# Kernel optimization log

Hardware: AMD Instinct MI355X
Metric: run time of the kernel (lower is better)

## Reference

```python
import jax, jax.numpy as jnp
import numpy as np


def _conv(x, w):
    # SpykeTorch snn.Convolution: plain conv2d, no bias, no padding (VALID)
    return jax.lax.conv_general_dilated(
        x, w, window_strides=(1, 1), padding='VALID',
        dimension_numbers=('NCHW', 'OIHW', 'NCHW'))


def _pad2(x, p=2):
    # sf.pad(input, pad=(2,2,2,2), value=0): zero-pad last two (spatial) dims
    return jnp.pad(x, ((0, 0), (0, 0), (p, p), (p, p)))


def _fire(pot, thr):
    # sf.fire: thresholded[pot <= thr] = 0 ; spk = thresholded.sign()
    thresholded = jnp.where(pot > thr, pot, jnp.zeros((), pot.dtype))
    spk = (pot > thr).astype(pot.dtype)
    return spk, thresholded


def _pool(x, k, s):
    # sf.pooling: max_pool2d, floor mode (== VALID reduce_window)
    return jax.lax.reduce_window(
        x, -jnp.inf, jax.lax.max,
        window_dimensions=(1, 1, k, k),
        window_strides=(1, 1, s, s),
        padding='VALID')


def setup_inputs() -> dict:
    key = jax.random.key(0)
    kx, k1, k2, k3 = jax.random.split(key, 4)
    # (T, C, H, W): T timesteps act as batch in SpykeTorch
    x = jax.random.uniform(kx, (20, 6, 160, 160), dtype=jnp.float32)

    def xavier_normal(k, shape):
        fan_in = shape[1] * shape[2] * shape[3]
        fan_out = shape[0] * shape[2] * shape[3]
        std = float(np.sqrt(2.0 / (fan_in + fan_out)))
        return jax.random.normal(k, shape, dtype=jnp.float32) * std

    w1 = xavier_normal(k1, (30, 6, 4, 4))
    w2 = xavier_normal(k2, (250, 30, 3, 3))
    w3 = xavier_normal(k3, (200, 250, 3, 3))
    return {'x': x, 'w1': w1, 'w2': w2, 'w3': w3, 'layer_idx': 3}


def reference(x, w1, w2, w3, layer_idx):
    # Eval-mode forward path of deepSNN up to `layer_idx` (tensor-returning branches)
    CONV1_T, CONV2_T, CONV3_T = 1.0, 1.0, 25.0
    inp = _pad2(x.astype(jnp.float32))          # (T,6,164,164)
    pot = _conv(inp, w1)                        # (T,30,161,161)
    spk, pot = _fire(pot, CONV1_T)
    if layer_idx == 1:
        return spk, pot
    pot = _conv(_pad2(_pool(spk, 2, 2)), w2)    # (T,250,82,82)
    spk, pot = _fire(pot, CONV2_T)
    if layer_idx == 2:
        return spk, pot
    pot = _conv(_pad2(_pool(spk, 3, 3)), w3)    # (T,200,29,29)
    spk, pot = _fire(pot, CONV3_T)
    return spk, pot
```

## Files before the change

kernel.cpp:

```cpp
#include <hip/hip_runtime.h>
#include <hip/hip_bf16.h>


#define OUT_HALF 3364000
#define MASK_PLANE 128000
#define T_FLOATS 168200

typedef float f32x16 __attribute__((ext_vector_type(16)));
typedef short bf8s __attribute__((ext_vector_type(8)));
typedef float f32x4 __attribute__((ext_vector_type(4)));
typedef f32x4 f32x4u __attribute__((aligned(4)));

static __device__ __forceinline__ unsigned int pkbf(float a, float b) {
    union { __hip_bfloat162 h; unsigned int u; } cv;
    cv.h = __float22bfloat162_rn(make_float2(a, b));
    return cv.u;
}
static __device__ __forceinline__ unsigned short bfbits(float a) {
    union { __hip_bfloat16 h; unsigned short u; } cv;
    cv.h = __float2bfloat16(a);
    return cv.u;
}

__global__ __launch_bounds__(256) void k_prep(const float* __restrict__ x,
                                              const float* __restrict__ w2,
                                              float* __restrict__ xpad,
                                              float* __restrict__ w2t,
                                              unsigned int* __restrict__ flags2) {
    int bidx = blockIdx.x;
    int tid = threadIdx.x;
    if (bidx >= 1576) {
        int tb = bidx - 1576;
        if (tb == 0)
            for (int i = tid; i < 540; i += 256) flags2[i] = 0u;
        int idx = tb * 256 + tid;
        if (idx < 67500) {
            int oc = idx / 270, ck = idx % 270;
            w2t[ck * 250 + oc] = w2[idx];
        }
        return;
    }
    for (int e = bidx * 256 + tid; e < 3227520; e += 403456) {
        int tc = e / 26896;
        int rem = e - tc * 26896;
        int r = rem / 164, col = rem - r * 164;
        int sr = r - 2, sc = col - 2;
        float v = 0.f;
        if ((unsigned)sr < 160u && (unsigned)sc < 160u)
            v = x[(tc * 160 + sr) * 160 + sc];
        xpad[e] = v;
    }
}

__global__ __launch_bounds__(256) void k_conv1m(const float* __restrict__ xpad,
                                                const float* __restrict__ w1,
                                                unsigned int* __restrict__ mask1) {
    __shared__ unsigned short B_lds[6 * 64 * 8];

    int tid = threadIdx.x;
#pragma unroll
    for (int n = 0; n < 12; ++n) {
        int q = n * 256 + tid;
        int i = q & 7, ll = (q >> 3) & 63, ks = q >> 9;
        int oc = ll & 31;
        int kg = ks * 16 + ((ll >> 5) << 3) + i;
        float w = (oc < 30) ? w1[oc * 96 + kg] : 0.f;
        B_lds[q] = bfbits(w);
    }
    __syncthreads();

    int l = tid & 63, wv = tid >> 6;
    int b = blockIdx.x;
    int t = b / 100;
    int u = (b % 100) * 4 + wv;
    int pr = u / 5, jblk = u % 5;
    int m = l & 31, hi = l >> 5;
    int j = jblk * 32 + m;

    bf8s bq[6];
#pragma unroll
    for (int ks = 0; ks < 6; ++ks)
        bq[ks] = *(const bf8s*)&B_lds[(ks * 64 + l) * 8];

    f32x16 acc0 = (f32x16)(0.0f);
    f32x16 acc1 = (f32x16)(0.0f);
    int r0 = 2 * pr + 2 * hi;

#pragma unroll
    for (int ks = 0; ks < 6; ++ks) {
        const float* base = xpad + ((t * 6 + ks) * 164 + r0) * 164 + j;
        f32x4 v0 = *(const f32x4u*)(base);
        f32x4 v1 = *(const f32x4u*)(base + 164);
        f32x4 v2 = *(const f32x4u*)(base + 328);
        union { bf8s s; unsigned int u4[4]; } a0, a1;
        a0.u4[0] = pkbf(v0.x, v0.y);
        a0.u4[1] = pkbf(v0.z, v0.w);
        a0.u4[2] = pkbf(v1.x, v1.y);
        a0.u4[3] = pkbf(v1.z, v1.w);
        a1.u4[0] = a0.u4[2];
        a1.u4[1] = a0.u4[3];
        a1.u4[2] = pkbf(v2.x, v2.y);
        a1.u4[3] = pkbf(v2.z, v2.w);
        acc0 = __builtin_amdgcn_mfma_f32_32x32x16_bf16(a0.s, bq[ks], acc0, 0, 0, 0);
        acc1 = __builtin_amdgcn_mfma_f32_32x32x16_bf16(a1.s, bq[ks], acc1, 0, 0, 0);
    }

    unsigned int mbase = (unsigned int)((t * 80 + pr) * 80 + jblk * 16);
#pragma unroll
    for (int a = 0; a < 8; ++a) {
        bool s = acc0[2 * a] > 1.f || acc0[2 * a + 1] > 1.f ||
                 acc1[2 * a] > 1.f || acc1[2 * a + 1] > 1.f;
        unsigned long long bal = __ballot(s);
        if (l < 6) {
            int h = l >> 1;
            unsigned int word = (l & 1) ? (unsigned int)(bal >> 32)
                                        : (unsigned int)bal;
            int pc = (a & 1) + ((a >> 1) << 2) + ((l & 1) << 1);
            mask1[h * MASK_PLANE + mbase + pc] = (word >> (10 * h)) & 0x3FFu;
        }
    }
}

__global__ __launch_bounds__(256) void k_conv2(const unsigned int* __restrict__ mask1,
                                               const float* __restrict__ w2t,
                                               unsigned long long* __restrict__ pool2m,
                                               unsigned int* __restrict__ flags2) {
    __shared__ unsigned int m_lds[5 * 84];
    __shared__ int f2;

    int b = blockIdx.x;
    int ninth = b % 9;  b /= 9;
    int ph = b % 27;
    int t = b / 27;
    int tid = threadIdx.x;
    int ocl = tid & 63, wv = tid >> 6;
    int r0 = 3 * ph - 2;
    int pwA = ninth * 3;

    if (tid == 0) f2 = 0;
    for (int idx = tid; idx < 420; idx += 256) {
        int r = idx / 84, col = idx % 84;
        int gr = r0 + r, gc = col - 2;
        unsigned int v = 0;
        if ((unsigned)gr < 80u && (unsigned)gc < 80u) {
            int i2 = (t * 80 + gr) * 80 + gc;
            v = mask1[i2] | (mask1[MASK_PLANE + i2] << 10) |
                (mask1[2 * MASK_PLANE + i2] << 20);
        }
        m_lds[idx] = v;
    }
    __syncthreads();

    int oc = wv * 64 + ocl;
    const float* wb = w2t + oc;
    bool valid = oc < 250;
    unsigned long long* prow = pool2m + ((t * 27 + ph) * 27) * 4 + wv;

    {
        int c0A = 3 * pwA, c0B = c0A + 3;
        unsigned int qA[25], qB[25];
#pragma unroll
        for (int dr = 0; dr < 5; ++dr)
#pragma unroll
            for (int ds = 0; ds < 5; ++ds) {
                qA[dr * 5 + ds] = m_lds[dr * 84 + c0A + ds];
                qB[dr * 5 + ds] = m_lds[dr * 84 + c0B + ds];
            }

        float accA[3][3], accB[3][3];
#pragma unroll
        for (int i = 0; i < 3; ++i)
#pragma unroll
            for (int j = 0; j < 3; ++j) { accA[i][j] = 0.f; accB[i][j] = 0.f; }

#pragma unroll
        for (int dr = 0; dr < 5; ++dr) {
#pragma unroll
            for (int ds = 0; ds < 5; ++ds) {
                unsigned int mA = qA[dr * 5 + ds];
                unsigned int mB = qB[dr * 5 + ds];
                while (mA | mB) {
                    bool hA = mA != 0, hB = mB != 0;
                    int cA = __builtin_ctz(mA | 0x40000000u);
                    int cB = __builtin_ctz(mB | 0x40000000u);
                    mA &= mA - 1;
                    mB &= mB - 1;
                    const float* pA = wb + cA * 2250;
                    const float* pB = wb + cB * 2250;
                    float vA[3][3], vB[3][3];
#pragma unroll
                    for (int i = 0; i < 3; ++i) {
                        if (dr - i < 0 || dr - i > 2) continue;
#pragma unroll
                        for (int j = 0; j < 3; ++j) {
                            if (ds - j < 0 || ds - j > 2) continue;
                            int off = ((dr - i) * 3 + (ds - j)) * 250;
                            vA[i][j] = pA[off];
                            vB[i][j] = pB[off];
                        }
                    }
#pragma unroll
                    for (int i = 0; i < 3; ++i) {
                        if (dr - i < 0 || dr - i > 2) continue;
#pragma unroll
                        for (int j = 0; j < 3; ++j) {
                            if (ds - j < 0 || ds - j > 2) continue;
                            accA[i][j] += hA ? vA[i][j] : 0.f;
                            accB[i][j] += hB ? vB[i][j] : 0.f;
                        }
                    }
                }
            }
        }

        bool sA = false, sB = false;
#pragma unroll
        for (int i = 0; i < 3; ++i)
#pragma unroll
            for (int j = 0; j < 3; ++j) {
                sA = sA || (accA[i][j] > 1.f);
                sB = sB || (accB[i][j] > 1.f);
            }
        unsigned long long bA = __ballot(sA && valid);
        unsigned long long bB = __ballot(sB && valid);
        if (ocl == 0) {
            prow[pwA * 4] = bA;
            prow[(pwA + 1) * 4] = bB;
        }
        if (bA | bB) f2 = 1;
    }

    {
        int pw = pwA + 2;
        int c0 = 3 * pw;
        unsigned int q[25];
#pragma unroll
        for (int dr = 0; dr < 5; ++dr)
#pragma unroll
            for (int ds = 0; ds < 5; ++ds)
                q[dr * 5 + ds] = m_lds[dr * 84 + c0 + ds];

        float acc[3][3];
#pragma unroll
        for (int i = 0; i < 3; ++i)
#pragma unroll
            for (int j = 0; j < 3; ++j) acc[i][j] = 0.f;

#pragma unroll
        for (int dr = 0; dr < 5; ++dr) {
#pragma unroll
            for (int ds = 0; ds < 5; ++ds) {
                unsigned int m = q[dr * 5 + ds];
                while (m) {
                    int c1 = __builtin_ctz(m); m &= m - 1;
                    bool has2 = (m != 0);
                    int c2 = c1;
                    if (has2) { c2 = __builtin_ctz(m); m &= m - 1; }
                    const float* p1 = wb + c1 * 2250;
                    const float* p2 = wb + c2 * 2250;
                    float v1[3][3], v2[3][3];
#pragma unroll
                    for (int i = 0; i < 3; ++i) {
                        if (dr - i < 0 || dr - i > 2) continue;
#pragma unroll
                        for (int j = 0; j < 3; ++j) {
                            if (ds - j < 0 || ds - j > 2) continue;
                            int off = ((dr - i) * 3 + (ds - j)) * 250;
                            v1[i][j] = p1[off];
                            v2[i][j] = p2[off];
                        }
                    }
#pragma unroll
                    for (int i = 0; i < 3; ++i) {
                        if (dr - i < 0 || dr - i > 2) continue;
#pragma unroll
                        for (int j = 0; j < 3; ++j) {
                            if (ds - j < 0 || ds - j > 2) continue;
                            acc[i][j] += v1[i][j];
                            acc[i][j] += has2 ? v2[i][j] : 0.f;
                        }
                    }
                }
            }
        }

        bool s = false;
#pragma unroll
        for (int i = 0; i < 3; ++i)
#pragma unroll
            for (int j = 0; j < 3; ++j) s = s || (acc[i][j] > 1.f);

        unsigned long long blt = __ballot(s && valid);
        if (ocl == 0) prow[pw * 4] = blt;
        if (blt) f2 = 1;
    }

    __syncthreads();
    if (tid == 0 && f2) flags2[t * 27 + ph] = 1u;
}

__global__ __launch_bounds__(320) void k_conv3(const unsigned long long* __restrict__ pool2m,
                                               const float* __restrict__ w3,
                                               float* __restrict__ out,
                                               const unsigned int* __restrict__ flags2) {
    __shared__ float w_lds[25 * 9 * 40];
    __shared__ float in_lds[25 * 4 * 34];

    int b = blockIdx.x;
    int rb = b % 15;  b /= 15;
    int ocg = b % 5;  b /= 5;
    int t = b;
    int oc0 = ocg * 40;
    int r0 = 2 * rb;
    int tid = threadIdx.x;
    int ocl = tid % 40, ct = tid / 40;

    {
        unsigned int fT = 0;
        const unsigned int* fp = flags2 + t * 27;
#pragma unroll
        for (int r = 0; r < 27; ++r) fT |= fp[r];
        if (fT == 0) {
            float4 z; z.x = 0.f; z.y = 0.f; z.z = 0.f; z.w = 0.f;
            float4* o0 = (float4*)(out + (size_t)t * T_FLOATS);
            float4* o1 = (float4*)(out + OUT_HALF + (size_t)t * T_FLOATS);
            int s = ocg * 15 + rb;
            int lo = s * 561;
            int hi = lo + 561; if (hi > 42050) hi = 42050;
            for (int i = lo + tid; i < hi; i += 320) {
                o0[i] = z;
                o1[i] = z;
            }
            return;
        }
    }

    {
        unsigned int f = 0;
        int rlo = r0 - 2; if (rlo < 0) rlo = 0;
        int rhi = r0 + 1; if (rhi > 26) rhi = 26;
        for (int r = rlo; r <= rhi; ++r) f |= flags2[t * 27 + r];
        if (f == 0) {
            int nrows = (r0 + 1 < 29) ? 2 : 1;
            int stride = 29 * nrows;
            int cnt = 40 * stride;
            for (int idx = tid; idx < cnt; idx += 320) {
                int o = idx / stride, rem = idx % stride;
                size_t base = (size_t)((t * 200 + oc0 + o) * 29 + r0) * 29 + rem;
                out[base] = 0.f;
                out[OUT_HALF + base] = 0.f;
            }
            return;
        }
    }

    float acc[2][4];
#pragma unroll
    for (int i = 0; i < 2; ++i)
#pragma unroll
        for (int j = 0; j < 4; ++j) acc[i][j] = 0.f;

    for (int chn = 0; chn < 10; ++chn) {
        int cc0 = chn * 25;
        for (int idx = tid; idx < 25 * 9 * 40; idx += 320) {
            int o = idx % 40, ck = idx / 40;
            int ckg = cc0 * 9 + ck;
            w_lds[idx] = w3[(size_t)(oc0 + o) * 2250 + ckg];
        }
        for (int idx = tid; idx < 25 * 4 * 34; idx += 320) {
            int col = idx % 34;
            int rem = idx / 34;
            int r = rem & 3, cl = rem >> 2;
            int gr = r0 + r - 2, gc = col - 2;
            float v = 0.f;
            if ((unsigned)gr < 27u && (unsigned)gc < 27u) {
                int c = cc0 + cl;
                unsigned long long wbits =
                    pool2m[((t * 27 + gr) * 27 + gc) * 4 + (c >> 6)];
                v = (float)((wbits >> (c & 63)) & 1ull);
            }
            in_lds[idx] = v;
        }
        __syncthreads();

        for (int cl = 0; cl < 25; ++cl) {
            float in[4][6];
#pragma unroll
            for (int r = 0; r < 4; ++r)
#pragma unroll
                for (int j = 0; j < 6; ++j)
                    in[r][j] = in_lds[(cl * 4 + r) * 34 + ct * 4 + j];
            const float* wp = &w_lds[cl * 360 + ocl];
#pragma unroll
            for (int k = 0; k < 9; ++k) {
                float w = wp[k * 40];
                int kh = k / 3, kw = k % 3;
#pragma unroll
                for (int i = 0; i < 2; ++i)
#pragma unroll
                    for (int j = 0; j < 4; ++j)
                        acc[i][j] += in[i + kh][j + kw] * w;
            }
        }
        __syncthreads();
    }

    {
        int oc = oc0 + ocl;
#pragma unroll
        for (int i = 0; i < 2; ++i) {
            int r = r0 + i;
            if (r < 29) {
#pragma unroll
                for (int j = 0; j < 4; ++j) {
                    int col = ct * 4 + j;
                    if (col < 29) {
                        float pot = acc[i][j];
                        bool s = pot > 25.f;
                        size_t base = ((size_t)((t * 200 + oc) * 29 + r)) * 29 + col;
                        out[base] = s ? 1.f : 0.f;
                        out[OUT_HALF + base] = s ? pot : 0.f;
                    }
                }
            }
        }
    }
}

extern "C" void kernel_launch(void* const* d_in, const int* in_sizes, int n_in,
                              void* d_out, int out_size, void* d_ws, size_t ws_size,
                              hipStream_t stream) {
    const float* x  = (const float*)d_in[0];
    const float* w1 = (const float*)d_in[1];
    const float* w2 = (const float*)d_in[2];
    const float* w3 = (const float*)d_in[3];
    float* out = (float*)d_out;

    unsigned int* mask1 = (unsigned int*)d_ws;
    unsigned long long* pool2m = (unsigned long long*)((char*)d_ws + 1536000);
    float* w2t = (float*)((char*)d_ws + 2002560);
    unsigned int* flags2 = (unsigned int*)((char*)d_ws + 2277376);
    float* xpad = (float*)((char*)d_ws + 4194304);

    k_prep<<<1840, 256, 0, stream>>>(x, w2, xpad, w2t, flags2);
    k_conv1m<<<2000, 256, 0, stream>>>(xpad, w1, mask1);
    k_conv2<<<20 * 27 * 9, 256, 0, stream>>>(mask1, w2t, pool2m, flags2);
    k_conv3<<<20 * 5 * 15, 320, 0, stream>>>(pool2m, w3, out, flags2);
}
```

Before: 127.1 us.

## Pack conv2 weights as fp16 pairs and split waves across output positions

Conv2 weights are converted to packed half2 (two output channels per 32-bit word) in the prep kernel, so each lane accumulates two channels with packed float2 adds and half the weight loads. Waves are reorganised: two waves cover all 256 channel slots for one group of positions (pair A/B) while the other two waves handle the third position, instead of every wave doing all three positions for 64 channels. Ballot results are bit-interleaved back into the original 64-bit channel-mask layout. The fp16 rounding of weights can flip threshold comparisons near the boundary, risking small correctness deviations, and the wave split may unbalance work between the two groups.

New measurement: 126.2 us. No clear change (-0.7%).

```diff
diff --git a/kernel.cpp b/kernel.cpp
--- a/kernel.cpp
+++ b/kernel.cpp
@@ -1,5 +1,6 @@
 #include <hip/hip_runtime.h>
 #include <hip/hip_bf16.h>
+#include <hip/hip_fp16.h>
 
 
 #define OUT_HALF 3364000
@@ -9,6 +10,7 @@
 typedef float f32x16 __attribute__((ext_vector_type(16)));
 typedef short bf8s __attribute__((ext_vector_type(8)));
 typedef float f32x4 __attribute__((ext_vector_type(4)));
+typedef float v2f __attribute__((ext_vector_type(2)));
 typedef f32x4 f32x4u __attribute__((aligned(4)));
 
 static __device__ __forceinline__ unsigned int pkbf(float a, float b) {
@@ -21,11 +23,26 @@
     cv.h = __float2bfloat16(a);
     return cv.u;
 }
+static __device__ __forceinline__ v2f up2(unsigned int u) {
+    union { unsigned int u32; __half2 h2; } cv; cv.u32 = u;
+    float2 f = __half22float2(cv.h2);
+    v2f r; r.x = f.x; r.y = f.y;
+    return r;
+}
+static __device__ __forceinline__ unsigned long long expand32(unsigned int v) {
+    unsigned long long x = v;
+    x = (x | (x << 16)) & 0x0000FFFF0000FFFFull;
+    x = (x | (x << 8))  & 0x00FF00FF00FF00FFull;
+    x = (x | (x << 4))  & 0x0F0F0F0F0F0F0F0Full;
+    x = (x | (x << 2))  & 0x3333333333333333ull;
+    x = (x | (x << 1))  & 0x5555555555555555ull;
+    return x;
+}
 
 __global__ __launch_bounds__(256) void k_prep(const float* __restrict__ x,
                                               const float* __restrict__ w2,
                                               float* __restrict__ xpad,
-                                              float* __restrict__ w2t,
+                                              unsigned int* __restrict__ w2h,
                                               unsigned int* __restrict__ flags2) {
     int bidx = blockIdx.x;
     int tid = threadIdx.x;
@@ -34,9 +51,15 @@
         if (tb == 0)
             for (int i = tid; i < 540; i += 256) flags2[i] = 0u;
         int idx = tb * 256 + tid;
-        if (idx < 67500) {
-            int oc = idx / 270, ck = idx % 270;
-            w2t[ck * 250 + oc] = w2[idx];
+        if (idx < 34560) {
+            int ck = idx >> 7, pl = idx & 127;
+            int oc0 = 2 * pl, oc1 = oc0 + 1;
+            float a = (oc0 < 250) ? w2[oc0 * 270 + ck] : 0.f;
+            float b = (oc1 < 250) ? w2[oc1 * 270 + ck] : 0.f;
+            union { __half2 h2; unsigned int u; } cv;
+            cv.h2.x = __float2half(a);
+            cv.h2.y = __float2half(b);
+            w2h[idx] = cv.u;
         }
         return;
     }
@@ -122,7 +145,7 @@
 }
 
 __global__ __launch_bounds__(256) void k_conv2(const unsigned int* __restrict__ mask1,
-                                               const float* __restrict__ w2t,
+                                               const unsigned int* __restrict__ w2h,
                                                unsigned long long* __restrict__ pool2m,
                                                unsigned int* __restrict__ flags2) {
     __shared__ unsigned int m_lds[5 * 84];
@@ -133,7 +156,8 @@
     int ph = b % 27;
     int t = b / 27;
     int tid = threadIdx.x;
-    int ocl = tid & 63, wv = tid >> 6;
+    int l = tid & 63, wv = tid >> 6;
+    int h = wv & 1, grp = wv >> 1;
     int r0 = 3 * ph - 2;
     int pwA = ninth * 3;
 
@@ -151,12 +175,11 @@
     }
     __syncthreads();
 
-    int oc = wv * 64 + ocl;
-    const float* wb = w2t + oc;
-    bool valid = oc < 250;
-    unsigned long long* prow = pool2m + ((t * 27 + ph) * 27) * 4 + wv;
-
-    {
+    const unsigned int* wb = w2h + h * 64 + l;
+    unsigned long long* prow = pool2m + ((t * 27 + ph) * 27) * 4 + 2 * h;
+    v2f z2 = (v2f)(0.f);
+
+    if (grp == 0) {
         int c0A = 3 * pwA, c0B = c0A + 3;
         unsigned int qA[25], qB[25];
 #pragma unroll
@@ -167,11 +190,11 @@
                 qB[dr * 5 + ds] = m_lds[dr * 84 + c0B + ds];
             }
 
-        float accA[3][3], accB[3][3];
+        v2f accA[3][3], accB[3][3];
 #pragma unroll
         for (int i = 0; i < 3; ++i)
 #pragma unroll
-            for (int j = 0; j < 3; ++j) { accA[i][j] = 0.f; accB[i][j] = 0.f; }
+            for (int j = 0; j < 3; ++j) { accA[i][j] = z2; accB[i][j] = z2; }
 
 #pragma unroll
         for (int dr = 0; dr < 5; ++dr) {
@@ -185,18 +208,18 @@
                     int cB = __builtin_ctz(mB | 0x40000000u);
                     mA &= mA - 1;
                     mB &= mB - 1;
-                    const float* pA = wb + cA * 2250;
-                    const float* pB = wb + cB * 2250;
-                    float vA[3][3], vB[3][3];
+                    const unsigned int* pA = wb + cA * 1152;
+                    const unsigned int* pB = wb + cB * 1152;
+                    unsigned int uA[3][3], uB[3][3];
 #pragma unroll
                     for (int i = 0; i < 3; ++i) {
                         if (dr - i < 0 || dr - i > 2) continue;
 #pragma unroll
                         for (int j = 0; j < 3; ++j) {
                             if (ds - j < 0 || ds - j > 2) continue;
-                            int off = ((dr - i) * 3 + (ds - j)) * 250;
-                            vA[i][j] = pA[off];
-                            vB[i][j] = pB[off];
+                            int off = ((dr - i) * 3 + (ds - j)) * 128;
+                            uA[i][j] = pA[off];
+                            uB[i][j] = pB[off];
                         }
                     }
 #pragma unroll
@@ -205,32 +228,42 @@
 #pragma unroll
                         for (int j = 0; j < 3; ++j) {
                             if (ds - j < 0 || ds - j > 2) continue;
-                            accA[i][j] += hA ? vA[i][j] : 0.f;
-                            accB[i][j] += hB ? vB[i][j] : 0.f;
+                            accA[i][j] += hA ? up2(uA[i][j]) : z2;
+                            accB[i][j] += hB ? up2(uB[i][j]) : z2;
                         }
                     }
                 }
             }
         }
 
-        bool sA = false, sB = false;
+        bool sA0 = false, sA1 = false, sB0 = false, sB1 = false;
 #pragma unroll
         for (int i = 0; i < 3; ++i)
 #pragma unroll
             for (int j = 0; j < 3; ++j) {
-                sA = sA || (accA[i][j] > 1.f);
-                sB = sB || (accB[i][j] > 1.f);
-            }
-        unsigned long long bA = __ballot(sA && valid);
-        unsigned long long bB = __ballot(sB && valid);
-        if (ocl == 0) {
-            prow[pwA * 4] = bA;
-            prow[(pwA + 1) * 4] = bB;
-        }
-        if (bA | bB) f2 = 1;
-    }
-
-    {
+                sA0 = sA0 || (accA[i][j].x > 1.f);
+                sA1 = sA1 || (accA[i][j].y > 1.f);
+                sB0 = sB0 || (accB[i][j].x > 1.f);
+                sB1 = sB1 || (accB[i][j].y > 1.f);
+            }
+        unsigned long long bA0 = __ballot(sA0), bA1 = __ballot(sA1);
+        unsigned long long bB0 = __ballot(sB0), bB1 = __ballot(sB1);
+        unsigned long long wA0 = expand32((unsigned int)bA0) |
+                                 (expand32((unsigned int)bA1) << 1);
+        unsigned long long wA1 = expand32((unsigned int)(bA0 >> 32)) |
+                                 (expand32((unsigned int)(bA1 >> 32)) << 1);
+        unsigned long long wB0 = expand32((unsigned int)bB0) |
+                                 (expand32((unsigned int)bB1) << 1);
+        unsigned long long wB1 = expand32((unsigned int)(bB0 >> 32)) |
+                                 (expand32((unsigned int)(bB1 >> 32)) << 1);
+        if (l == 0) {
+            prow[pwA * 4]           = wA0;
+            prow[pwA * 4 + 1]       = wA1;
+            prow[(pwA + 1) * 4]     = wB0;
+            prow[(pwA + 1) * 4 + 1] = wB1;
+        }
+        if (wA0 | wA1 | wB0 | wB1) f2 = 1;
+    } else {
         int pw = pwA + 2;
         int c0 = 3 * pw;
         unsigned int q[25];
@@ -240,11 +273,11 @@
             for (int ds = 0; ds < 5; ++ds)
                 q[dr * 5 + ds] = m_lds[dr * 84 + c0 + ds];
 
-        float acc[3][3];
+        v2f acc[3][3];
 #pragma unroll
         for (int i = 0; i < 3; ++i)
 #pragma unroll
-            for (int j = 0; j < 3; ++j) acc[i][j] = 0.f;
+            for (int j = 0; j < 3; ++j) acc[i][j] = z2;
 
 #pragma unroll
         for (int dr = 0; dr < 5; ++dr) {
@@ -256,18 +289,18 @@
                     bool has2 = (m != 0);
                     int c2 = c1;
                     if (has2) { c2 = __builtin_ctz(m); m &= m - 1; }
-                    const float* p1 = wb + c1 * 2250;
-                    const float* p2 = wb + c2 * 2250;
-                    float v1[3][3], v2[3][3];
+                    const unsigned int* p1 = wb + c1 * 1152;
+                    const unsigned int* p2 = wb + c2 * 1152;
+                    unsigned int u1[3][3], u2[3][3];
 #pragma unroll
                     for (int i = 0; i < 3; ++i) {
                         if (dr - i < 0 || dr - i > 2) continue;
 #pragma unroll
                         for (int j = 0; j < 3; ++j) {
                             if (ds - j < 0 || ds - j > 2) continue;
-                            int off = ((dr - i) * 3 + (ds - j)) * 250;
-                            v1[i][j] = p1[off];
-                            v2[i][j] = p2[off];
+                            int off = ((dr - i) * 3 + (ds - j)) * 128;
+                            u1[i][j] = p1[off];
+                            u2[i][j] = p2[off];
                         }
                     }
 #pragma unroll
@@ -276,23 +309,32 @@
 #pragma unroll
                         for (int j = 0; j < 3; ++j) {
                             if (ds - j < 0 || ds - j > 2) continue;
-                            acc[i][j] += v1[i][j];
-                            acc[i][j] += has2 ? v2[i][j] : 0.f;
+                            acc[i][j] += up2(u1[i][j]);
+                            acc[i][j] += has2 ? up2(u2[i][j]) : z2;
                         }
                     }
                 }
             }
         }
 
-        bool s = false;
+        bool s0 = false, s1 = false;
 #pragma unroll
         for (int i = 0; i < 3; ++i)
 #pragma unroll
-            for (int j = 0; j < 3; ++j) s = s || (acc[i][j] > 1.f);
-
-        unsigned long long blt = __ballot(s && valid);
-        if (ocl == 0) prow[pw * 4] = blt;
-        if (blt) f2 = 1;
+            for (int j = 0; j < 3; ++j) {
+                s0 = s0 || (acc[i][j].x > 1.f);
+                s1 = s1 || (acc[i][j].y > 1.f);
+            }
+        unsigned long long b0 = __ballot(s0), b1 = __ballot(s1);
+        unsigned long long w0 = expand32((unsigned int)b0) |
+                                (expand32((unsigned int)b1) << 1);
+        unsigned long long w1 = expand32((unsigned int)(b0 >> 32)) |
+                                (expand32((unsigned int)(b1 >> 32)) << 1);
+        if (l == 0) {
+            prow[pw * 4]     = w0;
+            prow[pw * 4 + 1] = w1;
+        }
+        if (w0 | w1) f2 = 1;
     }
 
     __syncthreads();
@@ -438,12 +480,12 @@
 
     unsigned int* mask1 = (unsigned int*)d_ws;
     unsigned long long* pool2m = (unsigned long long*)((char*)d_ws + 1536000);
-    float* w2t = (float*)((char*)d_ws + 2002560);
+    unsigned int* w2h = (unsigned int*)((char*)d_ws + 2002560);
     unsigned int* flags2 = (unsigned int*)((char*)d_ws + 2277376);
     float* xpad = (float*)((char*)d_ws + 4194304);
 
-    k_prep<<<1840, 256, 0, stream>>>(x, w2, xpad, w2t, flags2);
+    k_prep<<<1711, 256, 0, stream>>>(x, w2, xpad, w2h, flags2);
     k_conv1m<<<2000, 256, 0, stream>>>(xpad, w1, mask1);
-    k_conv2<<<20 * 27 * 9, 256, 0, stream>>>(mask1, w2t, pool2m, flags2);
+    k_conv2<<<20 * 27 * 9, 256, 0, stream>>>(mask1, w2h, pool2m, flags2);
     k_conv3<<<20 * 5 * 15, 320, 0, stream>>>(pool2m, w3, out, flags2);
 }
```
